# Performance work log

Hardware: AMD Instinct MI355X
Metric: run time of the kernel (lower is better)

Reference implementation:

```python
import jax, jax.numpy as jnp
import numpy as np

T, B, H, K = 512, 64, 512, 16  # seq_len, batch, hidden_size, num_tags


def setup_inputs() -> dict:
    key = jax.random.key(0)
    ks = jax.random.split(key, 8)
    hidden = jax.random.normal(ks[0], (T, B, H), dtype=jnp.float32)
    W1 = jax.random.normal(ks[1], (H, H), dtype=jnp.float32) / np.float32(np.sqrt(H))
    b1 = jnp.zeros((H,), jnp.float32)
    W2 = jax.random.normal(ks[2], (H, K), dtype=jnp.float32) / np.float32(np.sqrt(H))
    b2 = jnp.zeros((K,), jnp.float32)
    transition = jax.random.normal(ks[3], (K, K), dtype=jnp.float32)
    lens = jax.random.randint(ks[4], (B,), T // 2, T + 1)  # valid lengths in [T/2, T]
    tags = jax.random.randint(ks[5], (T, B), 0, K)
    return dict(hidden=hidden, W1=W1, b1=b1, W2=W2, b2=b2,
                transition=transition, lens=lens, tags=tags)


def reference(hidden, W1, b1, W2, b2, transition, lens, tags):
    # Emission MLP (dropout is identity in eval): Linear -> ReLU -> Linear
    h = jax.nn.relu(hidden @ W1 + b1)          # [T, B, H]
    em = h @ W2 + b2                           # [T, B, K]

    # ---- forward (partition) score: linear-chain logsumexp DP ----
    def step(alpha, e_t):
        # alpha: [B, K] over prev tags; transition[curr, prev]
        a = jax.nn.logsumexp(alpha[:, None, :] + transition[None, :, :], axis=-1) + e_t
        return a, a

    alpha0 = em[0]
    _, alphas = jax.lax.scan(step, alpha0, em[1:])
    alphas = jnp.concatenate([alpha0[None], alphas], axis=0)            # [T, B, K]
    last = jnp.take_along_axis(alphas, (lens - 1)[None, :, None], axis=0)[0]  # [B, K]
    fwd_score = jax.nn.logsumexp(last, axis=-1)                          # [B]

    # ---- gold path score ----
    em_path = jnp.take_along_axis(em, tags[:, :, None], axis=-1)[..., 0]  # [T, B]
    trans_path = transition[tags[1:], tags[:-1]]                          # [T-1, B]
    steps = em_path.at[1:].add(trans_path)
    cum = jnp.cumsum(steps, axis=0)                                       # [T, B]
    gold = jnp.take_along_axis(cum, (lens - 1)[None, :], axis=0)[0]       # [B]

    return (fwd_score - gold).sum()
```

## Files before the change

### kernel.cpp

```cpp
#include <hip/hip_runtime.h>
#include <hip/hip_bf16.h>

#define TT 512
#define BB 64
#define HH 512
#define KK 16

#define NCH 16
#define CST (TT / NCH)

typedef __attribute__((ext_vector_type(8))) short bf16x8;
typedef __attribute__((ext_vector_type(4))) short bf16x4;
typedef __attribute__((ext_vector_type(4))) float f32x4;

#define MFMA_K16(A, B, C) __builtin_amdgcn_mfma_f32_16x16x16bf16_1k(A, B, C, 0, 0, 0)

__device__ __forceinline__ unsigned short f2bf(float f) {
    union { __hip_bfloat16 h; unsigned short u; } cvt;
    cvt.h = __float2bfloat16(f);
    return cvt.u;
}

__device__ __forceinline__ short rne_bf(float x) {
    unsigned u = __float_as_uint(x);
    u += 0x7fffu + ((u >> 16) & 1u);
    return (short)(u >> 16);
}

__device__ __forceinline__ float bf2f(short s) {
    return __uint_as_float(((unsigned)(unsigned short)s) << 16);
}

__global__ void prep_kernel(const float* __restrict__ W1, const float* __restrict__ W2,
                            unsigned short* __restrict__ W1t, unsigned short* __restrict__ W2t,
                            float* __restrict__ out) {
    const int bi = blockIdx.x, tx = threadIdx.x;
    if (bi < 64) {
        __shared__ float Ls[64][65];
        const int ti = bi & 7, tj = bi >> 3;
        const int r0 = ti * 64, c0 = tj * 64;
        const int r = tx >> 4, c4 = (tx & 15) * 4;
#pragma unroll
        for (int i = 0; i < 4; ++i) {
            float4 v = *(const float4*)(W1 + (size_t)(r0 + r + 16 * i) * HH + c0 + c4);
            Ls[c4 + 0][r + 16 * i] = v.x;
            Ls[c4 + 1][r + 16 * i] = v.y;
            Ls[c4 + 2][r + 16 * i] = v.z;
            Ls[c4 + 3][r + 16 * i] = v.w;
        }
        __syncthreads();
        const int rn = tx >> 4, k4 = (tx & 15) * 4;
#pragma unroll
        for (int i = 0; i < 4; ++i) {
            const int n = rn + 16 * i;
            ushort4 o;
            o.x = f2bf(Ls[n][k4 + 0]);
            o.y = f2bf(Ls[n][k4 + 1]);
            o.z = f2bf(Ls[n][k4 + 2]);
            o.w = f2bf(Ls[n][k4 + 3]);
            *(ushort4*)(W1t + (size_t)(c0 + n) * HH + r0 + k4) = o;
        }
    } else {
        if (tx == 0) out[0] = 0.0f;
        for (int idx = tx; idx < 16 * HH; idx += 256) {
            const int n = idx >> 9, k = idx & 511;
            W2t[idx] = f2bf(W2[k * KK + n]);
        }
    }
}

__global__ __launch_bounds__(256, 2)
void em_kernel(const float* __restrict__ hidden, const unsigned short* __restrict__ W1t,
               const float* __restrict__ b1, const unsigned short* __restrict__ W2t,
               const float* __restrict__ b2, float* __restrict__ em) {
    __shared__ __align__(16) unsigned char stage[50432];
    unsigned short* const As = (unsigned short*)stage;
    unsigned short* const Bs = (unsigned short*)(stage + 5120);

    const int tx = threadIdx.x;
    const int w = tx >> 6, lane = tx & 63;
    const int q = lane >> 4, nl = lane & 15;
    const int row0 = blockIdx.x * 64;
    const int ar = tx >> 2, ac8 = (tx & 3) * 8;

    f32x4 acc[4][8];
#pragma unroll
    for (int mt = 0; mt < 4; ++mt)
#pragma unroll
        for (int nt = 0; nt < 8; ++nt) acc[mt][nt] = (f32x4){0.f, 0.f, 0.f, 0.f};

    for (int kt = 0; kt < 16; ++kt) {
        const int k0 = kt * 32;
        __syncthreads();
#pragma unroll
        for (int it = 0; it < 8; ++it) {
            const int c = it * 256 + tx;
            const int n = c >> 2, slot = c & 3;
            const int kc = slot ^ ((n >> 1) & 3);
            __builtin_amdgcn_global_load_lds(
                (const __attribute__((address_space(1))) void*)(W1t + (size_t)n * HH + k0 + kc * 8),
                (__attribute__((address_space(3))) void*)(Bs + c * 8), 16, 0, 0);
        }
        {
            const float* src = hidden + (size_t)(row0 + ar) * HH + k0 + ac8;
            float4 v0 = *(const float4*)(src);
            float4 v1 = *(const float4*)(src + 4);
            bf16x8 o;
            o[0] = (short)f2bf(v0.x); o[1] = (short)f2bf(v0.y);
            o[2] = (short)f2bf(v0.z); o[3] = (short)f2bf(v0.w);
            o[4] = (short)f2bf(v1.x); o[5] = (short)f2bf(v1.y);
            o[6] = (short)f2bf(v1.z); o[7] = (short)f2bf(v1.w);
            *(bf16x8*)(As + ar * 40 + ac8) = o;
        }
        __syncthreads();
        bf16x8 af[4];
#pragma unroll
        for (int mt = 0; mt < 4; ++mt)
            af[mt] = *(const bf16x8*)(As + (16 * mt + nl) * 40 + q * 8);
#pragma unroll
        for (int nt = 0; nt < 8; ++nt) {
            const int n = 128 * w + 16 * nt + nl;
            const int slot = q ^ ((n >> 1) & 3);
            bf16x8 bf = *(const bf16x8*)(Bs + n * 32 + slot * 8);
#pragma unroll
            for (int mt = 0; mt < 4; ++mt)
                acc[mt][nt] = __builtin_amdgcn_mfma_f32_16x16x32_bf16(af[mt], bf, acc[mt][nt], 0, 0, 0);
        }
    }

    __syncthreads();
    unsigned short* const Hb  = (unsigned short*)stage;
    unsigned short* const W2s = (unsigned short*)(stage + 33792);
#pragma unroll
    for (int i = tx; i < 1024; i += 256) {
        const int n = i >> 6, kc = i & 63;
        *(bf16x8*)(W2s + n * 520 + kc * 8) = *(const bf16x8*)(W2t + n * HH + kc * 8);
    }

    f32x4 acc2 = (f32x4){0.f, 0.f, 0.f, 0.f};
#pragma unroll
    for (int c = 0; c < 2; ++c) {
        if ((w >> 1) == c) {
#pragma unroll
            for (int nt = 0; nt < 8; ++nt) {
                const float bv = b1[128 * w + 16 * nt + nl];
#pragma unroll
                for (int mt = 0; mt < 4; ++mt) {
#pragma unroll
                    for (int r = 0; r < 4; ++r) {
                        float v = acc[mt][nt][r] + bv;
                        v = v > 0.f ? v : 0.f;
                        Hb[(16 * mt + q * 4 + r) * 264 + 128 * (w & 1) + 16 * nt + nl] = f2bf(v);
                    }
                }
            }
        }
        __syncthreads();
#pragma unroll
        for (int ks = 0; ks < 8; ++ks) {
            bf16x8 a2  = *(const bf16x8*)(Hb + (16 * w + nl) * 264 + ks * 32 + q * 8);
            bf16x8 b2f = *(const bf16x8*)(W2s + nl * 520 + c * 256 + ks * 32 + q * 8);
            acc2 = __builtin_amdgcn_mfma_f32_16x16x32_bf16(a2, b2f, acc2, 0, 0, 0);
        }
        __syncthreads();
    }
#pragma unroll
    for (int r = 0; r < 4; ++r) {
        const int row = row0 + 16 * w + q * 4 + r;
        em[(size_t)row * KK + nl] = acc2[r] + b2[nl];
    }
}

__global__ void scan_gold_kernel(const float* __restrict__ em, const float* __restrict__ trans,
                                 const int* __restrict__ lens, const int* __restrict__ tags,
                                 float* __restrict__ Pfull, float* __restrict__ Cfull,
                                 float* __restrict__ Ppart, float* __restrict__ Cpart,
                                 float* __restrict__ out) {
    __shared__ float trs[256];
    __shared__ float red[4];
    const int tx = threadIdx.x;

    if (blockIdx.x >= 256) {
        trs[tx] = __logf(bf2f(rne_bf(__expf(trans[tx]))));
        __syncthreads();
        const int idx = (blockIdx.x - 256) * 256 + tx;
        const int t = idx >> 6, b = idx & 63;
        const int L = lens[b];
        float v = 0.0f;
        if (t < L) {
            const int tg = tags[t * BB + b];
            v = em[((size_t)t * BB + b) * KK + tg];
            if (t > 0) v += trs[tg * 16 + tags[(t - 1) * BB + b]];
        }
#pragma unroll
        for (int dd = 1; dd < 64; dd <<= 1) v += __shfl_xor(v, dd, 64);
        if ((tx & 63) == 0) red[tx >> 6] = v;
        __syncthreads();
        if (tx == 0) atomicAdd(out, -(red[0] + red[1] + red[2] + red[3]));
        return;
    }

    const int id = blockIdx.x * 4 + (tx >> 6);
    const int lane = tx & 63, q = lane >> 4, col = lane & 15;
    const int b = id >> 4, c = id & 15;

    float mf[4];
    {
        float4 tv = *(const float4*)(trans + col * 16 + 4 * q);
        mf[0] = bf2f(rne_bf(__expf(tv.x)));
        mf[1] = bf2f(rne_bf(__expf(tv.y)));
        mf[2] = bf2f(rne_bf(__expf(tv.z)));
        mf[3] = bf2f(rne_bf(__expf(tv.w)));
    }
    const int Lm1 = lens[b] - 1;
    const int tb0 = CST * c;

    float ebuf[8];
#pragma unroll
    for (int i = 0; i < 8; ++i)
        ebuf[i] = em[(size_t)((tb0 + i) * BB + b) * KK + col];

    bf16x4 gb;
#pragma unroll
    for (int i = 0; i < 4; ++i)
        gb[i] = (4 * q + i == col) ? rne_bf(1.0f) : (short)0;

    const f32x4 zc = (f32x4){0.f, 0.f, 0.f, 0.f};
    f32x4 d = (f32x4){0.f, 0.f, 0.f, 0.f};
    float K = 1.0f, rk = 1.0f, lk = 0.0f, Cacc = 0.0f;

    for (int sb = 0; sb < CST; sb += 8) {
        const bool refill = (sb < CST - 8);
#pragma unroll
        for (int s8 = 0; s8 < 8; ++s8) {
            const int t = tb0 + sb + s8;
            const float eraw = ebuf[s8];
            if (refill)
                ebuf[s8] = em[(size_t)((t + 8) * BB + b) * KK + col];
            float ev = __expf(eraw);
            if ((s8 & 3) == 0 && (sb + s8) >= 4) {
                ev *= rk;
                Cacc += lk;
            }
            bf16x4 af;
            af[0] = rne_bf(ev * mf[0]); af[1] = rne_bf(ev * mf[1]);
            af[2] = rne_bf(ev * mf[2]); af[3] = rne_bf(ev * mf[3]);
            if (s8 == 0) {
                if (sb == 0 && c == 0) {
#pragma unroll
                    for (int i = 0; i < 4; ++i)
                        af[i] = (4 * q + i == col) ? rne_bf(ev) : (short)0;
                }
            }
            d = MFMA_K16(af, gb, zc);
            if ((s8 & 3) == 1) {
                K = __shfl(d[0], 0, 64);
                const float Km = fmaxf(K, 1e-30f);
                rk = 1.0f / Km;
                lk = __logf(Km);
            }
            if (t == Lm1) {
#pragma unroll
                for (int r = 0; r < 4; ++r)
                    Ppart[b * 256 + (4 * q + r) * 16 + col] = d[r];
                if (lane == 0) Cpart[b] = Cacc;
            }
            gb[0] = rne_bf(d[0]); gb[1] = rne_bf(d[1]);
            gb[2] = rne_bf(d[2]); gb[3] = rne_bf(d[3]);
        }
    }
#pragma unroll
    for (int r = 0; r < 4; ++r)
        Pfull[(size_t)(b * NCH + c) * 256 + (4 * q + r) * 16 + col] = d[r];
    if (lane == 0) Cfull[b * NCH + c] = Cacc;
}

__global__ void combine_kernel(const int* __restrict__ lens,
                               const float* __restrict__ Pfull, const float* __restrict__ Cfull,
                               const float* __restrict__ Ppart, const float* __restrict__ Cpart,
                               float* __restrict__ out) {
    const int lane = threadIdx.x;
    const int grp = lane >> 4, j = lane & 15;
    const int b = blockIdx.x * 4 + grp;
    const int base = grp << 4;
    const int cstar = (lens[b] - 1) / CST;

    float g = 1.0f, acc = 0.0f;
    for (int c = 0; c < NCH; ++c) {
        const bool act = (c <= cstar);
        const float* P = (c < cstar) ? (Pfull + (size_t)(b * NCH + c) * 256)
                                     : (Ppart + b * 256);
        float gn = 0.0f;
#pragma unroll
        for (int k = 0; k < 16; ++k) {
            const float gk = __shfl(g, base + k, 64);
            gn += P[j * 16 + k] * gk;
        }
        if (act) {
            float m = gn;
#pragma unroll
            for (int dd = 1; dd < 16; dd <<= 1) m = fmaxf(m, __shfl_xor(m, dd, 64));
            g = gn / m;
            acc += __logf(m) + ((c < cstar) ? Cfull[b * NCH + c] : Cpart[b]);
        }
    }
    float ssum = g;
#pragma unroll
    for (int dd = 1; dd < 16; dd <<= 1) ssum += __shfl_xor(ssum, dd, 64);
    const float fwd = acc + __logf(ssum);
    if (j == 0) atomicAdd(out, fwd);
}

extern "C" void kernel_launch(void* const* d_in, const int* in_sizes, int n_in,
                              void* d_out, int out_size, void* d_ws, size_t ws_size,
                              hipStream_t stream) {
    const float* hidden = (const float*)d_in[0];
    const float* W1     = (const float*)d_in[1];
    const float* b1     = (const float*)d_in[2];
    const float* W2     = (const float*)d_in[3];
    const float* b2     = (const float*)d_in[4];
    const float* trans  = (const float*)d_in[5];
    const int*   lens   = (const int*)d_in[6];
    const int*   tags   = (const int*)d_in[7];
    float* out = (float*)d_out;

    char* ws = (char*)d_ws;
    float* em = (float*)ws;
    unsigned short* W1t = (unsigned short*)(ws + 2097152);
    unsigned short* W2t = (unsigned short*)(ws + 2621440);
    float* Pfull = (float*)(ws + 2637824);
    float* Cfull = (float*)(ws + 3686400);
    float* Ppart = (float*)(ws + 3690496);
    float* Cpart = (float*)(ws + 3756032);

    prep_kernel<<<65, 256, 0, stream>>>(W1, W2, W1t, W2t, out);
    em_kernel<<<512, 256, 0, stream>>>(hidden, W1t, b1, W2t, b2, em);
    scan_gold_kernel<<<384, 256, 0, stream>>>(em, trans, lens, tags,
                                              Pfull, Cfull, Ppart, Cpart, out);
    combine_kernel<<<16, 64, 0, stream>>>(lens, Pfull, Cfull, Ppart, Cpart, out);
}
```

Measured before the change: 148.1 us.

## Split em GEMM hidden dimension across two blocks with atomic accumulation

The emission MLP kernel now splits the 512 hidden columns into two halves, so each block computes a 64x256 tile of the first GEMM and a partial second GEMM, then atomically adds its result into em. The prep kernel zeroes em first, and launch bounds rise to 4 blocks per CU because each block needs less LDS and fewer accumulator registers. This doubles the grid to improve occupancy and latency hiding. In exchange, each 64-row hidden tile is loaded and converted twice, and float atomics make the summation order nondeterministic.

```diff
diff --git a/kernel.cpp b/kernel.cpp
--- a/kernel.cpp
+++ b/kernel.cpp
@@ -33,7 +33,7 @@
 
 __global__ void prep_kernel(const float* __restrict__ W1, const float* __restrict__ W2,
                             unsigned short* __restrict__ W1t, unsigned short* __restrict__ W2t,
-                            float* __restrict__ out) {
+                            float* __restrict__ em, float* __restrict__ out) {
     const int bi = blockIdx.x, tx = threadIdx.x;
     if (bi < 64) {
         __shared__ float Ls[64][65];
@@ -60,45 +60,52 @@
             o.w = f2bf(Ls[n][k4 + 3]);
             *(ushort4*)(W1t + (size_t)(c0 + n) * HH + r0 + k4) = o;
         }
-    } else {
+    } else if (bi == 64) {
         if (tx == 0) out[0] = 0.0f;
         for (int idx = tx; idx < 16 * HH; idx += 256) {
             const int n = idx >> 9, k = idx & 511;
             W2t[idx] = f2bf(W2[k * KK + n]);
         }
-    }
-}
-
-__global__ __launch_bounds__(256, 2)
+    } else {
+        float4* dst = (float4*)(em + (size_t)(bi - 65) * 4096);
+        const float4 z = {0.f, 0.f, 0.f, 0.f};
+#pragma unroll
+        for (int i = 0; i < 4; ++i) dst[tx + 256 * i] = z;
+    }
+}
+
+__global__ __launch_bounds__(256, 4)
 void em_kernel(const float* __restrict__ hidden, const unsigned short* __restrict__ W1t,
                const float* __restrict__ b1, const unsigned short* __restrict__ W2t,
                const float* __restrict__ b2, float* __restrict__ em) {
-    __shared__ __align__(16) unsigned char stage[50432];
+    __shared__ __align__(16) unsigned char stage[33792];
     unsigned short* const As = (unsigned short*)stage;
     unsigned short* const Bs = (unsigned short*)(stage + 5120);
 
     const int tx = threadIdx.x;
     const int w = tx >> 6, lane = tx & 63;
     const int q = lane >> 4, nl = lane & 15;
-    const int row0 = blockIdx.x * 64;
+    const int rb = blockIdx.x & 511, nh = blockIdx.x >> 9;
+    const int row0 = rb * 64;
+    const int ncol0 = nh * 256;
     const int ar = tx >> 2, ac8 = (tx & 3) * 8;
 
-    f32x4 acc[4][8];
+    f32x4 acc[4][4];
 #pragma unroll
     for (int mt = 0; mt < 4; ++mt)
 #pragma unroll
-        for (int nt = 0; nt < 8; ++nt) acc[mt][nt] = (f32x4){0.f, 0.f, 0.f, 0.f};
+        for (int nt = 0; nt < 4; ++nt) acc[mt][nt] = (f32x4){0.f, 0.f, 0.f, 0.f};
 
     for (int kt = 0; kt < 16; ++kt) {
         const int k0 = kt * 32;
         __syncthreads();
 #pragma unroll
-        for (int it = 0; it < 8; ++it) {
+        for (int it = 0; it < 4; ++it) {
             const int c = it * 256 + tx;
             const int n = c >> 2, slot = c & 3;
             const int kc = slot ^ ((n >> 1) & 3);
             __builtin_amdgcn_global_load_lds(
-                (const __attribute__((address_space(1))) void*)(W1t + (size_t)n * HH + k0 + kc * 8),
+                (const __attribute__((address_space(1))) void*)(W1t + (size_t)(ncol0 + n) * HH + k0 + kc * 8),
                 (__attribute__((address_space(3))) void*)(Bs + c * 8), 16, 0, 0);
         }
         {
@@ -118,8 +125,8 @@
         for (int mt = 0; mt < 4; ++mt)
             af[mt] = *(const bf16x8*)(As + (16 * mt + nl) * 40 + q * 8);
 #pragma unroll
-        for (int nt = 0; nt < 8; ++nt) {
-            const int n = 128 * w + 16 * nt + nl;
+        for (int nt = 0; nt < 4; ++nt) {
+            const int n = 64 * w + 16 * nt + nl;
             const int slot = q ^ ((n >> 1) & 3);
             bf16x8 bf = *(const bf16x8*)(Bs + n * 32 + slot * 8);
 #pragma unroll
@@ -129,45 +136,36 @@
     }
 
     __syncthreads();
-    unsigned short* const Hb  = (unsigned short*)stage;
-    unsigned short* const W2s = (unsigned short*)(stage + 33792);
-#pragma unroll
-    for (int i = tx; i < 1024; i += 256) {
-        const int n = i >> 6, kc = i & 63;
-        *(bf16x8*)(W2s + n * 520 + kc * 8) = *(const bf16x8*)(W2t + n * HH + kc * 8);
-    }
-
+    unsigned short* const Hb = (unsigned short*)stage;
+#pragma unroll
+    for (int nt = 0; nt < 4; ++nt) {
+        const float bv = b1[ncol0 + 64 * w + 16 * nt + nl];
+#pragma unroll
+        for (int mt = 0; mt < 4; ++mt) {
+#pragma unroll
+            for (int r = 0; r < 4; ++r) {
+                float v = acc[mt][nt][r] + bv;
+                v = v > 0.f ? v : 0.f;
+                Hb[(16 * mt + q * 4 + r) * 264 + 64 * w + 16 * nt + nl] = f2bf(v);
+            }
+        }
+    }
+    bf16x8 b2f[8];
+#pragma unroll
+    for (int ks = 0; ks < 8; ++ks)
+        b2f[ks] = *(const bf16x8*)(W2t + (size_t)nl * HH + ncol0 + ks * 32 + q * 8);
+    __syncthreads();
     f32x4 acc2 = (f32x4){0.f, 0.f, 0.f, 0.f};
 #pragma unroll
-    for (int c = 0; c < 2; ++c) {
-        if ((w >> 1) == c) {
-#pragma unroll
-            for (int nt = 0; nt < 8; ++nt) {
-                const float bv = b1[128 * w + 16 * nt + nl];
-#pragma unroll
-                for (int mt = 0; mt < 4; ++mt) {
-#pragma unroll
-                    for (int r = 0; r < 4; ++r) {
-                        float v = acc[mt][nt][r] + bv;
-                        v = v > 0.f ? v : 0.f;
-                        Hb[(16 * mt + q * 4 + r) * 264 + 128 * (w & 1) + 16 * nt + nl] = f2bf(v);
-                    }
-                }
-            }
-        }
-        __syncthreads();
-#pragma unroll
-        for (int ks = 0; ks < 8; ++ks) {
-            bf16x8 a2  = *(const bf16x8*)(Hb + (16 * w + nl) * 264 + ks * 32 + q * 8);
-            bf16x8 b2f = *(const bf16x8*)(W2s + nl * 520 + c * 256 + ks * 32 + q * 8);
-            acc2 = __builtin_amdgcn_mfma_f32_16x16x32_bf16(a2, b2f, acc2, 0, 0, 0);
-        }
-        __syncthreads();
+    for (int ks = 0; ks < 8; ++ks) {
+        bf16x8 a2 = *(const bf16x8*)(Hb + (16 * w + nl) * 264 + ks * 32 + q * 8);
+        acc2 = __builtin_amdgcn_mfma_f32_16x16x32_bf16(a2, b2f[ks], acc2, 0, 0, 0);
     }
 #pragma unroll
     for (int r = 0; r < 4; ++r) {
         const int row = row0 + 16 * w + q * 4 + r;
-        em[(size_t)row * KK + nl] = acc2[r] + b2[nl];
+        const float val = acc2[r] + (nh == 0 ? b2[nl] : 0.0f);
+        atomicAdd(&em[(size_t)row * KK + nl], val);
     }
 }
 
@@ -333,8 +331,8 @@
     float* Ppart = (float*)(ws + 3690496);
     float* Cpart = (float*)(ws + 3756032);
 
-    prep_kernel<<<65, 256, 0, stream>>>(W1, W2, W1t, W2t, out);
-    em_kernel<<<512, 256, 0, stream>>>(hidden, W1t, b1, W2t, b2, em);
+    prep_kernel<<<193, 256, 0, stream>>>(W1, W2, W1t, W2t, em, out);
+    em_kernel<<<1024, 256, 0, stream>>>(hidden, W1t, b1, W2t, b2, em);
     scan_gold_kernel<<<384, 256, 0, stream>>>(em, trans, lens, tags,
                                               Pfull, Cfull, Ppart, Cpart, out);
     combine_kernel<<<16, 64, 0, stream>>>(lens, Pfull, Cfull, Ppart, Cpart, out);
```

Result: slower. 159.6 us (+7.8%).

## Double-buffer W1 tiles, preload full A block, and use 512-thread em blocks

Applied to the files above, without the earlier changes.

The emission GEMM kernel now loads the whole 64x512 hidden tile into LDS as bf16 once up front, instead of one k-slice per iteration. W1 k-slices are double-buffered so the next slice is fetched asynchronously while the current one is being multiplied, which removes one barrier per iteration. Blocks grow to 512 threads in a 2x4 wave grid, with fewer accumulators per wave. LDS use rises to about 129KB, so only one block fits per CU and occupancy drops in exchange for the overlap.

```diff
diff --git a/kernel.cpp b/kernel.cpp
--- a/kernel.cpp
+++ b/kernel.cpp
@@ -69,40 +69,43 @@
     }
 }
 
-__global__ __launch_bounds__(256, 2)
+__global__ __launch_bounds__(512, 1)
 void em_kernel(const float* __restrict__ hidden, const unsigned short* __restrict__ W1t,
                const float* __restrict__ b1, const unsigned short* __restrict__ W2t,
                const float* __restrict__ b2, float* __restrict__ em) {
-    __shared__ __align__(16) unsigned char stage[50432];
-    unsigned short* const As = (unsigned short*)stage;
-    unsigned short* const Bs = (unsigned short*)(stage + 5120);
+    __shared__ __align__(16) unsigned char stage[132096];
+    unsigned short* const As  = (unsigned short*)stage;
+    unsigned short* const Bs0 = (unsigned short*)(stage + 66560);
+    unsigned short* const Bs1 = (unsigned short*)(stage + 99328);
 
     const int tx = threadIdx.x;
     const int w = tx >> 6, lane = tx & 63;
     const int q = lane >> 4, nl = lane & 15;
+    const int wm = w >> 2, wn = w & 3;
     const int row0 = blockIdx.x * 64;
-    const int ar = tx >> 2, ac8 = (tx & 3) * 8;
-
-    f32x4 acc[4][8];
-#pragma unroll
-    for (int mt = 0; mt < 4; ++mt)
-#pragma unroll
-        for (int nt = 0; nt < 8; ++nt) acc[mt][nt] = (f32x4){0.f, 0.f, 0.f, 0.f};
-
-    for (int kt = 0; kt < 16; ++kt) {
-        const int k0 = kt * 32;
-        __syncthreads();
+
+#define ISSUE_B(KT, BDST)                                                                 \
+    {                                                                                     \
+        const int k0b = (KT) * 32;                                                        \
+        _Pragma("unroll")                                                                 \
+        for (int it = 0; it < 4; ++it) {                                                  \
+            const int c = it * 512 + tx;                                                  \
+            const int n = c >> 2, slot = c & 3;                                           \
+            const int kc = slot ^ ((n >> 1) & 3);                                         \
+            __builtin_amdgcn_global_load_lds(                                             \
+                (const __attribute__((address_space(1))) void*)(W1t + (size_t)n * HH + k0b + kc * 8), \
+                (__attribute__((address_space(3))) void*)((BDST) + c * 8), 16, 0, 0);     \
+        }                                                                                 \
+    }
+
+    ISSUE_B(0, Bs0);
+    {
+        const int arow = tx >> 3;
+        const int acb  = (tx & 7) * 8;
 #pragma unroll
         for (int it = 0; it < 8; ++it) {
-            const int c = it * 256 + tx;
-            const int n = c >> 2, slot = c & 3;
-            const int kc = slot ^ ((n >> 1) & 3);
-            __builtin_amdgcn_global_load_lds(
-                (const __attribute__((address_space(1))) void*)(W1t + (size_t)n * HH + k0 + kc * 8),
-                (__attribute__((address_space(3))) void*)(Bs + c * 8), 16, 0, 0);
-        }
-        {
-            const float* src = hidden + (size_t)(row0 + ar) * HH + k0 + ac8;
+            const int col = it * 64 + acb;
+            const float* src = hidden + (size_t)(row0 + arow) * HH + col;
             float4 v0 = *(const float4*)(src);
             float4 v1 = *(const float4*)(src + 4);
             bf16x8 o;
@@ -110,20 +113,31 @@
             o[2] = (short)f2bf(v0.z); o[3] = (short)f2bf(v0.w);
             o[4] = (short)f2bf(v1.x); o[5] = (short)f2bf(v1.y);
             o[6] = (short)f2bf(v1.z); o[7] = (short)f2bf(v1.w);
-            *(bf16x8*)(As + ar * 40 + ac8) = o;
-        }
-        __syncthreads();
-        bf16x8 af[4];
-#pragma unroll
-        for (int mt = 0; mt < 4; ++mt)
-            af[mt] = *(const bf16x8*)(As + (16 * mt + nl) * 40 + q * 8);
+            *(bf16x8*)(As + arow * 520 + col) = o;
+        }
+    }
+
+    f32x4 acc[2][8];
+#pragma unroll
+    for (int mt = 0; mt < 2; ++mt)
+#pragma unroll
+        for (int nt = 0; nt < 8; ++nt) acc[mt][nt] = (f32x4){0.f, 0.f, 0.f, 0.f};
+
+    for (int kt = 0; kt < 16; ++kt) {
+        __syncthreads();
+        if (kt < 15) ISSUE_B(kt + 1, (kt & 1) ? Bs0 : Bs1);
+        unsigned short* const Bs = (kt & 1) ? Bs1 : Bs0;
+        bf16x8 af[2];
+#pragma unroll
+        for (int mt = 0; mt < 2; ++mt)
+            af[mt] = *(const bf16x8*)(As + (32 * wm + 16 * mt + nl) * 520 + kt * 32 + q * 8);
 #pragma unroll
         for (int nt = 0; nt < 8; ++nt) {
-            const int n = 128 * w + 16 * nt + nl;
+            const int n = 128 * wn + 16 * nt + nl;
             const int slot = q ^ ((n >> 1) & 3);
             bf16x8 bf = *(const bf16x8*)(Bs + n * 32 + slot * 8);
 #pragma unroll
-            for (int mt = 0; mt < 4; ++mt)
+            for (int mt = 0; mt < 2; ++mt)
                 acc[mt][nt] = __builtin_amdgcn_mfma_f32_16x16x32_bf16(af[mt], bf, acc[mt][nt], 0, 0, 0);
         }
     }
@@ -132,7 +146,7 @@
     unsigned short* const Hb  = (unsigned short*)stage;
     unsigned short* const W2s = (unsigned short*)(stage + 33792);
 #pragma unroll
-    for (int i = tx; i < 1024; i += 256) {
+    for (int i = tx; i < 1024; i += 512) {
         const int n = i >> 6, kc = i & 63;
         *(bf16x8*)(W2s + n * 520 + kc * 8) = *(const bf16x8*)(W2t + n * HH + kc * 8);
     }
@@ -140,35 +154,40 @@
     f32x4 acc2 = (f32x4){0.f, 0.f, 0.f, 0.f};
 #pragma unroll
     for (int c = 0; c < 2; ++c) {
-        if ((w >> 1) == c) {
+        if ((wn >> 1) == c) {
 #pragma unroll
             for (int nt = 0; nt < 8; ++nt) {
-                const float bv = b1[128 * w + 16 * nt + nl];
-#pragma unroll
-                for (int mt = 0; mt < 4; ++mt) {
+                const float bv = b1[128 * wn + 16 * nt + nl];
+#pragma unroll
+                for (int mt = 0; mt < 2; ++mt) {
 #pragma unroll
                     for (int r = 0; r < 4; ++r) {
                         float v = acc[mt][nt][r] + bv;
                         v = v > 0.f ? v : 0.f;
-                        Hb[(16 * mt + q * 4 + r) * 264 + 128 * (w & 1) + 16 * nt + nl] = f2bf(v);
+                        Hb[(32 * wm + 16 * mt + q * 4 + r) * 264 + 128 * (wn & 1) + 16 * nt + nl] = f2bf(v);
                     }
                 }
             }
         }
         __syncthreads();
-#pragma unroll
-        for (int ks = 0; ks < 8; ++ks) {
-            bf16x8 a2  = *(const bf16x8*)(Hb + (16 * w + nl) * 264 + ks * 32 + q * 8);
-            bf16x8 b2f = *(const bf16x8*)(W2s + nl * 520 + c * 256 + ks * 32 + q * 8);
-            acc2 = __builtin_amdgcn_mfma_f32_16x16x32_bf16(a2, b2f, acc2, 0, 0, 0);
-        }
-        __syncthreads();
-    }
-#pragma unroll
-    for (int r = 0; r < 4; ++r) {
-        const int row = row0 + 16 * w + q * 4 + r;
-        em[(size_t)row * KK + nl] = acc2[r] + b2[nl];
-    }
+        if (w < 4) {
+#pragma unroll
+            for (int ks = 0; ks < 8; ++ks) {
+                bf16x8 a2  = *(const bf16x8*)(Hb + (16 * w + nl) * 264 + ks * 32 + q * 8);
+                bf16x8 b2f = *(const bf16x8*)(W2s + nl * 520 + c * 256 + ks * 32 + q * 8);
+                acc2 = __builtin_amdgcn_mfma_f32_16x16x32_bf16(a2, b2f, acc2, 0, 0, 0);
+            }
+        }
+        __syncthreads();
+    }
+    if (w < 4) {
+#pragma unroll
+        for (int r = 0; r < 4; ++r) {
+            const int row = row0 + 16 * w + q * 4 + r;
+            em[(size_t)row * KK + nl] = acc2[r] + b2[nl];
+        }
+    }
+#undef ISSUE_B
 }
 
 __global__ void scan_gold_kernel(const float* __restrict__ em, const float* __restrict__ trans,
@@ -334,7 +353,7 @@
     float* Cpart = (float*)(ws + 3756032);
 
     prep_kernel<<<65, 256, 0, stream>>>(W1, W2, W1t, W2t, out);
-    em_kernel<<<512, 256, 0, stream>>>(hidden, W1t, b1, W2t, b2, em);
+    em_kernel<<<512, 512, 0, stream>>>(hidden, W1t, b1, W2t, b2, em);
     scan_gold_kernel<<<384, 256, 0, stream>>>(em, trans, lens, tags,
                                               Pfull, Cfull, Ppart, Cpart, out);
     combine_kernel<<<16, 64, 0, stream>>>(lens, Pfull, Cfull, Ppart, Cpart, out);
```

New measurement: 148.2 us. No clear change (+0.1%).
